# Kernel tuning notes

Hardware: AMD Instinct MI355X
Metric: run time of the kernel (lower is better)

Reference implementation:

```python
import jax, jax.numpy as jnp
import numpy as np

H = 8            # num_heads
EPS = 1e-5       # LayerNorm eps (torch default)
SLOPE = 0.01     # leaky_relu negative slope (torch default)


def layernorm(x, g, b):
    mu = jnp.mean(x, axis=-1, keepdims=True)
    var = jnp.mean((x - mu) ** 2, axis=-1, keepdims=True)
    return (x - mu) * jax.lax.rsqrt(var + EPS) * g + b


def setup_inputs() -> dict:
    key = jax.random.key(0)
    ks = jax.random.split(key, 20)
    B, T, Din, Dh = 4, 2048, 512, 512
    s_in = 1.0 / np.sqrt(Din)
    s_h = 1.0 / np.sqrt(Dh)
    inp = {
        'q': jax.random.normal(ks[0], (B, T, Din), jnp.float32),
        'k': jax.random.normal(ks[1], (B, T, Din), jnp.float32),
        'v': jax.random.normal(ks[2], (B, T, Din), jnp.float32),
        # attention projections (stored as [in, out] for x @ W + b)
        'Wq': jax.random.uniform(ks[3], (Din, Dh), jnp.float32, -s_in, s_in),
        'bq': jax.random.uniform(ks[4], (Dh,), jnp.float32, -s_in, s_in),
        'Wk': jax.random.uniform(ks[5], (Din, Dh), jnp.float32, -s_in, s_in),
        'bk': jax.random.uniform(ks[6], (Dh,), jnp.float32, -s_in, s_in),
        'Wv': jax.random.uniform(ks[7], (Din, Dh), jnp.float32, -s_in, s_in),
        'bv': jax.random.uniform(ks[8], (Dh,), jnp.float32, -s_in, s_in),
        'Wo': jax.random.uniform(ks[9], (Dh, Dh), jnp.float32, -s_h, s_h),
        'bo': jax.random.uniform(ks[10], (Dh,), jnp.float32, -s_h, s_h),
        # FFN
        'Wh': jax.random.uniform(ks[11], (Dh, Dh), jnp.float32, -s_h, s_h),
        'bh': jax.random.uniform(ks[12], (Dh,), jnp.float32, -s_h, s_h),
        'W2': jax.random.uniform(ks[13], (Dh, Dh), jnp.float32, -s_h, s_h),
        'b2': jax.random.uniform(ks[14], (Dh,), jnp.float32, -s_h, s_h),
        # LayerNorms
        'g1': jnp.ones((Dh,), jnp.float32),
        'be1': jnp.zeros((Dh,), jnp.float32),
        'g2': jnp.ones((Dh,), jnp.float32),
        'be2': jnp.zeros((Dh,), jnp.float32),
    }
    return inp


def _block(q, k, v, Wq, bq, Wk, bk, Wv, bv, Wo, bo, Wh, bh, W2, b2, g1, be1, g2, be2):
    B, Tq, _ = q.shape
    Tk = k.shape[1]
    Dh = Wq.shape[1]
    dh = Dh // H
    # projections -> [B, H, T, dh]
    qh = (q @ Wq + bq).reshape(B, Tq, H, dh).transpose(0, 2, 1, 3)
    kh = (k @ Wk + bk).reshape(B, Tk, H, dh).transpose(0, 2, 1, 3)
    vh = (v @ Wv + bv).reshape(B, Tk, H, dh).transpose(0, 2, 1, 3)
    scores = jnp.einsum('bhqd,bhkd->bhqk', qh, kh) / np.sqrt(dh)
    # causal mask: tril with diagonal = Tk - Tq (matches get_causal_mask)
    mask = jnp.tril(jnp.ones((Tq, Tk), bool), k=Tk - Tq)
    scores = jnp.where(mask, scores, -jnp.inf)
    attn = jax.nn.softmax(scores, axis=-1)
    x = jnp.einsum('bhqk,bhkd->bhqd', attn, vh)
    x = x.transpose(0, 2, 1, 3).reshape(B, Tq, Dh)
    h = x @ Wo + bo
    if h.shape == q.shape:
        h = h + q  # residual
    h = layernorm(h, g1, be1)
    y = jax.nn.leaky_relu(h @ Wh + bh, SLOPE) @ W2 + b2
    y = y + h  # residual (shapes always equal here)
    return layernorm(y, g2, be2)


def reference(q, k, v, Wq, bq, Wk, bk, Wv, bv, Wo, bo, Wh, bh, W2, b2, g1, be1, g2, be2):
    return _block(q, k, v, Wq, bq, Wk, bk, Wv, bv, Wo, bo, Wh, bh, W2, b2, g1, be1, g2, be2)
```

## Files before the change

### kernel.cpp

```cpp
#include <hip/hip_runtime.h>
#include <math.h>

#define DIN   512
#define TSEQ  2048
#define BATCH 4
#define NH    8
#define DHEAD 64
#define MTOT  8192

typedef __attribute__((ext_vector_type(8))) __bf16 bf16x8;
typedef __attribute__((ext_vector_type(8))) short  s16x8;
typedef __attribute__((ext_vector_type(4))) float  f32x4;

__device__ __forceinline__ unsigned short f2b(float f) {
  union { float f; unsigned int u; } c; c.f = f;
  unsigned int r = (c.u + 0x7fffu + ((c.u >> 16) & 1u)) >> 16;
  return (unsigned short)r;
}

__device__ __forceinline__ unsigned int pkbf(float a, float b) {
  union { __bf16 h[2]; unsigned int u; } c;
  c.h[0] = (__bf16)a; c.h[1] = (__bf16)b; return c.u;
}

__device__ __forceinline__ f32x4 mfma16(bf16x8 a, bf16x8 b, f32x4 c) {
  return __builtin_amdgcn_mfma_f32_16x16x32_bf16(a, b, c, 0, 0, 0);
}

__device__ __forceinline__ void gload16(const void* gsrc, void* ldsbase) {
  __builtin_amdgcn_global_load_lds(
      (const __attribute__((address_space(1))) unsigned int*)gsrc,
      (__attribute__((address_space(3))) unsigned int*)(unsigned int)(unsigned long long)ldsbase,
      16, 0, 0);
}

#define VMCNT0_BARRIER() do { \
    asm volatile("s_waitcnt vmcnt(0)" ::: "memory"); \
    __builtin_amdgcn_s_barrier(); } while (0)

__global__ __launch_bounds__(256) void cast3_kernel(const float* __restrict__ q,
                                                    const float* __restrict__ k,
                                                    const float* __restrict__ v,
                                                    unsigned short* __restrict__ oq,
                                                    unsigned short* __restrict__ ok,
                                                    unsigned short* __restrict__ ov) {
  const float* in = blockIdx.y == 0 ? q : blockIdx.y == 1 ? k : v;
  unsigned short* out = blockIdx.y == 0 ? oq : blockIdx.y == 1 ? ok : ov;
  int i = (blockIdx.x * 256 + threadIdx.x) * 8;
  float4 a = *(const float4*)(in + i);
  float4 b = *(const float4*)(in + i + 4);
  ushort4 u0, u1;
  u0.x = f2b(a.x); u0.y = f2b(a.y); u0.z = f2b(a.z); u0.w = f2b(a.w);
  u1.x = f2b(b.x); u1.y = f2b(b.y); u1.z = f2b(b.z); u1.w = f2b(b.w);
  *(ushort4*)(out + i) = u0;
  *(ushort4*)(out + i + 4) = u1;
}

__global__ __launch_bounds__(256) void transpose6_kernel(const float* __restrict__ w0,
                                                         const float* __restrict__ w1,
                                                         const float* __restrict__ w2,
                                                         const float* __restrict__ w3,
                                                         const float* __restrict__ w4,
                                                         const float* __restrict__ w5,
                                                         unsigned short* __restrict__ Wt) {
  const float* W;
  switch (blockIdx.z) {
    case 0: W = w0; break; case 1: W = w1; break; case 2: W = w2; break;
    case 3: W = w3; break; case 4: W = w4; break; default: W = w5; break;
  }
  unsigned short* dst = Wt + (size_t)blockIdx.z * 512 * 512;
  __shared__ float tile[32][33];
  int bx = blockIdx.x * 32, by = blockIdx.y * 32;
  int tx = threadIdx.x & 31, ty = threadIdx.x >> 5;
  #pragma unroll
  for (int yy = ty; yy < 32; yy += 8)
    tile[yy][tx] = W[(size_t)(by + yy) * DIN + bx + tx];
  __syncthreads();
  #pragma unroll
  for (int yy = ty; yy < 32; yy += 8)
    dst[(size_t)(bx + yy) * DIN + by + tx] = f2b(tile[tx][yy]);
}

__device__ __forceinline__ void gemm_core(const unsigned short* __restrict__ A,
                                          const unsigned short* __restrict__ Bt,
                                          int m0, int n0,
                                          unsigned short (*Als)[64 * 64],
                                          unsigned short (*Bls)[128 * 64],
                                          f32x4 (*acc)[4]) {
  const int tid = threadIdx.x, lane = tid & 63, w = tid >> 6;
  const int wr = w >> 1, wc = w & 1;
  const int l = lane & 15, g = lane >> 4;
  const int r8 = lane >> 3;
  const int sce = ((lane & 7) ^ r8) * 8;
  const int sxr = (l & 7) * 8;

  #define GSTAGE(buf, k0) do { \
      _Pragma("unroll") \
      for (int i_ = 0; i_ < 2; ++i_) { \
        int ia_ = w * 2 + i_; \
        gload16(A + (size_t)(m0 + ia_ * 8 + r8) * 512 + (k0) + sce, &Als[buf][ia_ * 512]); \
      } \
      _Pragma("unroll") \
      for (int i_ = 0; i_ < 4; ++i_) { \
        int ib_ = w * 4 + i_; \
        gload16(Bt + (size_t)(n0 + ib_ * 8 + r8) * 512 + (k0) + sce, &Bls[buf][ib_ * 512]); \
      } } while (0)

  GSTAGE(0, 0);
  VMCNT0_BARRIER();
  for (int t = 0; t < 8; ++t) {
    int cur = t & 1;
    if (t < 7) GSTAGE(cur ^ 1, (t + 1) * 64);
    #pragma unroll
    for (int kk = 0; kk < 2; ++kk) {
      bf16x8 af[2], bf[4];
      #pragma unroll
      for (int m = 0; m < 2; ++m)
        af[m] = *(const bf16x8*)(&Als[cur][(wr * 32 + m * 16 + l) * 64 + ((kk * 32 + g * 8) ^ sxr)]);
      #pragma unroll
      for (int n = 0; n < 4; ++n)
        bf[n] = *(const bf16x8*)(&Bls[cur][(wc * 64 + n * 16 + l) * 64 + ((kk * 32 + g * 8) ^ sxr)]);
      #pragma unroll
      for (int m = 0; m < 2; ++m)
        #pragma unroll
        for (int n = 0; n < 4; ++n)
          acc[m][n] = mfma16(af[m], bf[n], acc[m][n]);
    }
    VMCNT0_BARRIER();
  }
  #undef GSTAGE
}

enum { EPI_BF16 = 0, EPI_F32RES = 2, EPI_LRELU = 3 };

template <int EPI>
__global__ __launch_bounds__(256) void gemm_kernel(const unsigned short* __restrict__ A,
                                                   const unsigned short* __restrict__ Bt,
                                                   const float* __restrict__ bias,
                                                   const float* __restrict__ res,
                                                   void* __restrict__ out) {
  __shared__ unsigned short Als[2][64 * 64];
  __shared__ unsigned short Bls[2][128 * 64];
  const int lane = threadIdx.x & 63, w = threadIdx.x >> 6;
  const int wr = w >> 1, wc = w & 1;
  const int l = lane & 15, g = lane >> 4;
  const int m0 = blockIdx.x * 64, n0 = blockIdx.y * 128;
  f32x4 acc[2][4] = {};
  gemm_core(A, Bt, m0, n0, Als, Bls, acc);

  #pragma unroll
  for (int m = 0; m < 2; ++m) {
    int grb = m0 + wr * 32 + m * 16 + g * 4;
    #pragma unroll
    for (int n = 0; n < 4; ++n) {
      int gc = n0 + wc * 64 + n * 16 + l;
      float bv = bias[gc];
      #pragma unroll
      for (int r = 0; r < 4; ++r) {
        int gr = grb + r;
        float v = acc[m][n][r] + bv;
        if (EPI == EPI_F32RES) {
          ((float*)out)[(size_t)gr * 512 + gc] = v + res[(size_t)gr * 512 + gc];
        } else if (EPI == EPI_BF16) {
          ((unsigned short*)out)[(size_t)gr * 512 + gc] = f2b(v);
        } else {
          v = v > 0.f ? v : 0.01f * v;
          ((unsigned short*)out)[(size_t)gr * 512 + gc] = f2b(v);
        }
      }
    }
  }
}

__global__ __launch_bounds__(256) void gemm_qkv_kernel(const unsigned short* __restrict__ qb,
                                                       const unsigned short* __restrict__ kb,
                                                       const unsigned short* __restrict__ vb,
                                                       const unsigned short* __restrict__ Wt,
                                                       const float* __restrict__ bq,
                                                       const float* __restrict__ bk,
                                                       const float* __restrict__ bv,
                                                       unsigned short* __restrict__ Qp,
                                                       unsigned short* __restrict__ Kp,
                                                       unsigned short* __restrict__ Vt) {
  __shared__ unsigned short Als[2][64 * 64];
  __shared__ unsigned short Bls[2][128 * 64];
  const int z = blockIdx.z;
  const unsigned short* A = z == 0 ? qb : z == 1 ? kb : vb;
  const unsigned short* B = Wt + (size_t)z * 512 * 512;
  const float* bias = z == 0 ? bq : z == 1 ? bk : bv;
  const int lane = threadIdx.x & 63, w = threadIdx.x >> 6;
  const int wr = w >> 1, wc = w & 1;
  const int l = lane & 15, g = lane >> 4;
  const int m0 = blockIdx.x * 64, n0 = blockIdx.y * 128;
  f32x4 acc[2][4] = {};
  gemm_core(A, B, m0, n0, Als, Bls, acc);

  #pragma unroll
  for (int m = 0; m < 2; ++m) {
    int grb = m0 + wr * 32 + m * 16 + g * 4;
    #pragma unroll
    for (int n = 0; n < 4; ++n) {
      int gc = n0 + wc * 64 + n * 16 + l;
      float bvl = bias[gc];
      #pragma unroll
      for (int r = 0; r < 4; ++r) {
        int gr = grb + r;
        float v = acc[m][n][r] + bvl;
        if (z == 0) {
          Qp[(size_t)gr * 512 + gc] = f2b(v);
        } else if (z == 1) {
          Kp[(size_t)gr * 512 + gc] = f2b(v);
        } else {
          int b = gr >> 11, t = gr & 2047;
          Vt[((size_t)(b * 512 + gc) << 11) + t] = f2b(v);
        }
      }
    }
  }
}

__global__ __launch_bounds__(256) void attn_kernel(const unsigned short* __restrict__ Q,
                                                   const unsigned short* __restrict__ K,
                                                   const unsigned short* __restrict__ Vt,
                                                   unsigned short* __restrict__ O) {
  __shared__ unsigned short Kls[2][64 * 64];
  __shared__ unsigned short Vls[2][64 * 64];
  __shared__ unsigned short Pls[4][16 * 64];
  const int tid = threadIdx.x, lane = tid & 63, w = tid >> 6;
  const int l = lane & 15, g = lane >> 4;
  const int bh = blockIdx.x;
  const int qt = (int)gridDim.y - 1 - (int)blockIdx.y;
  const int b = bh >> 3, h = bh & 7;
  const int sx = (l & 7) * 8;
  const float SC2 = 0.125f * 1.44269504088896340736f;
  const float THR = 64.f;

  const int r8 = lane >> 3;
  const int sce = ((lane & 7) ^ r8) * 8;

  #define STAGEKV(buf, kv0) do { \
      _Pragma("unroll") \
      for (int i_ = 0; i_ < 2; ++i_) { \
        int ii_ = w * 2 + i_; \
        int row_ = ii_ * 8 + r8; \
        gload16(K  + (size_t)(b * 2048 + (kv0) + row_) * 512 + h * 64 + sce, &Kls[buf][ii_ * 512]); \
        gload16(Vt + (size_t)(b * 512 + h * 64 + row_) * 2048 + (kv0) + sce, &Vls[buf][ii_ * 512]); \
      } } while (0)

  const int q0 = qt * 64 + w * 16;
  bf16x8 qf[2];
  #pragma unroll
  for (int kf = 0; kf < 2; ++kf)
    qf[kf] = *(const bf16x8*)(Q + (size_t)(b * 2048 + q0 + l) * 512 + h * 64 + kf * 32 + g * 8);

  bf16x8 vones;
  #pragma unroll
  for (int i = 0; i < 8; ++i) vones[i] = (__bf16)1.0f;

  float mrun = -1e30f;
  f32x4 o[4] = {};
  f32x4 os = {0.f, 0.f, 0.f, 0.f};

  STAGEKV(0, 0);
  VMCNT0_BARRIER();

  for (int s = 0; s <= qt; ++s) {
    int cur = s & 1;
    if (s < qt) STAGEKV(cur ^ 1, (s + 1) * 64);
    int kv0 = s * 64;

    f32x4 st[4];
    #pragma unroll
    for (int t = 0; t < 4; ++t) {
      st[t] = f32x4{0.f, 0.f, 0.f, 0.f};
      #pragma unroll
      for (int kf = 0; kf < 2; ++kf) {
        bf16x8 kfr = *(const bf16x8*)(&Kls[cur][(t * 16 + l) * 64 + ((kf * 32 + g * 8) ^ sx)]);
        st[t] = mfma16(kfr, qf[kf], st[t]);
      }
    }
    if (s == qt) {
      const int qrow = q0 + l;
      #pragma unroll
      for (int t = 0; t < 4; ++t)
        #pragma unroll
        for (int r = 0; r < 4; ++r)
          if (kv0 + t * 16 + g * 4 + r > qrow) st[t][r] = -1e30f;
    }

    float mx = fmaxf(
        fmaxf(fmaxf(fmaxf(st[0][0], st[0][1]), st[0][2]),
              fmaxf(fmaxf(st[0][3], st[1][0]), st[1][1])),
        fmaxf(fmaxf(fmaxf(st[1][2], st[1][3]), st[2][0]),
              fmaxf(fmaxf(st[2][1], st[2][2]), st[2][3])));
    mx = fmaxf(mx, fmaxf(fmaxf(st[3][0], st[3][1]), fmaxf(st[3][2], st[3][3])));
    mx = fmaxf(mx, __shfl_xor(mx, 16, 64));
    mx = fmaxf(mx, __shfl_xor(mx, 32, 64));

    if (!__all(mx <= mrun + THR)) {
      float nm = fmaxf(mrun, mx);
      float alpha = exp2f((mrun - nm) * SC2);
      mrun = nm;
      #pragma unroll
      for (int r = 0; r < 4; ++r) {
        float ar = __shfl(alpha, g * 4 + r, 64);
        #pragma unroll
        for (int n = 0; n < 4; ++n) o[n][r] *= ar;
        os[r] *= ar;
      }
    }

    float mS = mrun * SC2;
    #pragma unroll
    for (int t = 0; t < 4; ++t)
      #pragma unroll
      for (int r = 0; r < 4; ++r)
        st[t][r] = exp2f(fmaf(st[t][r], SC2, -mS));

    #pragma unroll
    for (int t = 0; t < 4; ++t) {
      uint2 u;
      u.x = pkbf(st[t][0], st[t][1]);
      u.y = pkbf(st[t][2], st[t][3]);
      *(uint2*)(&Pls[w][l * 64 + ((t * 16 + g * 4) ^ sx)]) = u;
    }
    #pragma unroll
    for (int kf = 0; kf < 2; ++kf) {
      bf16x8 pa = *(const bf16x8*)(&Pls[w][l * 64 + ((kf * 32 + g * 8) ^ sx)]);
      #pragma unroll
      for (int n = 0; n < 4; ++n) {
        bf16x8 vf = *(const bf16x8*)(&Vls[cur][(n * 16 + l) * 64 + ((kf * 32 + g * 8) ^ sx)]);
        o[n] = mfma16(pa, vf, o[n]);
      }
      os = mfma16(pa, vones, os);
    }

    VMCNT0_BARRIER();
  }

  #pragma unroll
  for (int r = 0; r < 4; ++r) {
    float lir = 1.f / os[r];
    #pragma unroll
    for (int n = 0; n < 4; ++n)
      O[(size_t)(b * 2048 + q0 + g * 4 + r) * 512 + h * 64 + n * 16 + l] =
          f2b(o[n][r] * lir);
  }
  #undef STAGEKV
}

template <int WRITE_BF16>
__global__ __launch_bounds__(256) void ln_kernel(const float* __restrict__ X,
                                                 const float* __restrict__ g,
                                                 const float* __restrict__ be,
                                                 float* __restrict__ Yf,
                                                 unsigned short* __restrict__ Yb) {
  int row = blockIdx.x * 4 + (threadIdx.x >> 6);
  int lane = threadIdx.x & 63;
  const float* x = X + (size_t)row * 512;
  float4 v0 = *(const float4*)(x + lane * 4);
  float4 v1 = *(const float4*)(x + 256 + lane * 4);
  float s = v0.x + v0.y + v0.z + v0.w + v1.x + v1.y + v1.z + v1.w;
  #pragma unroll
  for (int t = 1; t < 64; t <<= 1) s += __shfl_xor(s, t, 64);
  float mu = s * (1.f / 512.f);
  float q = 0.f;
  q += (v0.x - mu) * (v0.x - mu); q += (v0.y - mu) * (v0.y - mu);
  q += (v0.z - mu) * (v0.z - mu); q += (v0.w - mu) * (v0.w - mu);
  q += (v1.x - mu) * (v1.x - mu); q += (v1.y - mu) * (v1.y - mu);
  q += (v1.z - mu) * (v1.z - mu); q += (v1.w - mu) * (v1.w - mu);
  #pragma unroll
  for (int t = 1; t < 64; t <<= 1) q += __shfl_xor(q, t, 64);
  float rstd = rsqrtf(q * (1.f / 512.f) + 1e-5f);

  float4 g0 = *(const float4*)(g + lane * 4);
  float4 g1 = *(const float4*)(g + 256 + lane * 4);
  float4 b0 = *(const float4*)(be + lane * 4);
  float4 b1 = *(const float4*)(be + 256 + lane * 4);
  float4 y0, y1;
  y0.x = (v0.x - mu) * rstd * g0.x + b0.x; y0.y = (v0.y - mu) * rstd * g0.y + b0.y;
  y0.z = (v0.z - mu) * rstd * g0.z + b0.z; y0.w = (v0.w - mu) * rstd * g0.w + b0.w;
  y1.x = (v1.x - mu) * rstd * g1.x + b1.x; y1.y = (v1.y - mu) * rstd * g1.y + b1.y;
  y1.z = (v1.z - mu) * rstd * g1.z + b1.z; y1.w = (v1.w - mu) * rstd * g1.w + b1.w;
  if (Yf) {
    *(float4*)(Yf + (size_t)row * 512 + lane * 4) = y0;
    *(float4*)(Yf + (size_t)row * 512 + 256 + lane * 4) = y1;
  }
  if (WRITE_BF16) {
    ushort4 u0, u1;
    u0.x = f2b(y0.x); u0.y = f2b(y0.y); u0.z = f2b(y0.z); u0.w = f2b(y0.w);
    u1.x = f2b(y1.x); u1.y = f2b(y1.y); u1.z = f2b(y1.z); u1.w = f2b(y1.w);
    *(ushort4*)(Yb + (size_t)row * 512 + lane * 4) = u0;
    *(ushort4*)(Yb + (size_t)row * 512 + 256 + lane * 4) = u1;
  }
}

extern "C" void kernel_launch(void* const* d_in, const int* in_sizes, int n_in,
                              void* d_out, int out_size, void* d_ws, size_t ws_size,
                              hipStream_t stream) {
  const float* q_in = (const float*)d_in[0];
  const float* k_in = (const float*)d_in[1];
  const float* v_in = (const float*)d_in[2];
  const float* Wq = (const float*)d_in[3];  const float* bq = (const float*)d_in[4];
  const float* Wk = (const float*)d_in[5];  const float* bk = (const float*)d_in[6];
  const float* Wv = (const float*)d_in[7];  const float* bv = (const float*)d_in[8];
  const float* Wo = (const float*)d_in[9];  const float* bo = (const float*)d_in[10];
  const float* Wh = (const float*)d_in[11]; const float* bh = (const float*)d_in[12];
  const float* W2 = (const float*)d_in[13]; const float* b2 = (const float*)d_in[14];
  const float* g1 = (const float*)d_in[15]; const float* be1 = (const float*)d_in[16];
  const float* g2 = (const float*)d_in[17]; const float* be2 = (const float*)d_in[18];

  char* ws = (char*)d_ws;
  const size_t MD2 = (size_t)MTOT * 512 * 2;
  const size_t W1  = (size_t)512 * 512 * 2;
  const size_t MD4 = (size_t)MTOT * 512 * 4;
  unsigned short* qb_  = (unsigned short*)(ws);
  unsigned short* kb_  = (unsigned short*)(ws + MD2);
  unsigned short* vb_  = (unsigned short*)(ws + 2 * MD2);
  unsigned short* Qp   = (unsigned short*)(ws + 3 * MD2);
  unsigned short* Kp   = (unsigned short*)(ws + 4 * MD2);
  unsigned short* Vt   = (unsigned short*)(ws + 5 * MD2);
  unsigned short* Wt   = (unsigned short*)(ws + 6 * MD2);
  float*          hy   = (float*)(ws + 6 * MD2 + 6 * W1);
  float*          ln1f = (float*)(ws + 6 * MD2 + 6 * W1 + MD4);
  unsigned short* attn = vb_;
  unsigned short* ln1b = qb_;
  unsigned short* f1   = kb_;

  cast3_kernel<<<dim3(MTOT * 512 / 2048, 3), 256, 0, stream>>>(q_in, k_in, v_in, qb_, kb_, vb_);
  transpose6_kernel<<<dim3(16, 16, 6), 256, 0, stream>>>(Wq, Wk, Wv, Wo, Wh, W2, Wt);

  gemm_qkv_kernel<<<dim3(MTOT / 64, 4, 3), 256, 0, stream>>>(
      qb_, kb_, vb_, Wt, bq, bk, bv, Qp, Kp, Vt);

  attn_kernel<<<dim3(BATCH * NH, 32), 256, 0, stream>>>(Qp, Kp, Vt, attn);

  dim3 gg(MTOT / 64, 4);
  gemm_kernel<EPI_F32RES><<<gg, 256, 0, stream>>>(attn, Wt + 3 * 512 * 512, bo, q_in, hy);
  ln_kernel<1><<<MTOT / 4, 256, 0, stream>>>(hy, g1, be1, ln1f, ln1b);
  gemm_kernel<EPI_LRELU><<<gg, 256, 0, stream>>>(ln1b, Wt + 4 * 512 * 512, bh, nullptr, f1);
  gemm_kernel<EPI_F32RES><<<gg, 256, 0, stream>>>(f1, Wt + 5 * 512 * 512, b2, ln1f, hy);
  ln_kernel<0><<<MTOT / 4, 256, 0, stream>>>(hy, g2, be2, (float*)d_out, nullptr);
}
```

Baseline: 255.9 us.

## Shrink GEMM tiles, keep intermediates in bf16, load V directly from global in attention

GEMM tiles go from 64x128 with K-step 64 to 64x64 with K-step 32, which doubles the grid and cuts LDS use, and the XOR swizzle is removed. Intermediates before and after each LayerNorm are now stored as bf16 instead of fp32, and the second residual reads the bf16 LN1 output, which reduces memory traffic and accuracy. The attention kernel stops staging V through LDS and reads V fragments straight from global memory. Without the swizzle the LDS reads may hit bank conflicts, and the unstaged V loads may stall the MFMA work.

After: 297.0 us. 1.16x slower.

```diff
diff --git a/kernel.cpp b/kernel.cpp
--- a/kernel.cpp
+++ b/kernel.cpp
@@ -16,6 +16,10 @@
   union { float f; unsigned int u; } c; c.f = f;
   unsigned int r = (c.u + 0x7fffu + ((c.u >> 16) & 1u)) >> 16;
   return (unsigned short)r;
+}
+
+__device__ __forceinline__ float b2f(unsigned short u) {
+  union { unsigned int i; float f; } c; c.i = (unsigned int)u << 16; return c.f;
 }
 
 __device__ __forceinline__ unsigned int pkbf(float a, float b) {
@@ -84,88 +88,78 @@
 __device__ __forceinline__ void gemm_core(const unsigned short* __restrict__ A,
                                           const unsigned short* __restrict__ Bt,
                                           int m0, int n0,
-                                          unsigned short (*Als)[64 * 64],
-                                          unsigned short (*Bls)[128 * 64],
-                                          f32x4 (*acc)[4]) {
+                                          unsigned short (*Als)[64 * 32],
+                                          unsigned short (*Bls)[64 * 32],
+                                          f32x4 (*acc)[2]) {
   const int tid = threadIdx.x, lane = tid & 63, w = tid >> 6;
   const int wr = w >> 1, wc = w & 1;
   const int l = lane & 15, g = lane >> 4;
-  const int r8 = lane >> 3;
-  const int sce = ((lane & 7) ^ r8) * 8;
-  const int sxr = (l & 7) * 8;
+  const int srow = lane >> 2;
+  const int sce  = (lane & 3) * 8;
 
   #define GSTAGE(buf, k0) do { \
-      _Pragma("unroll") \
-      for (int i_ = 0; i_ < 2; ++i_) { \
-        int ia_ = w * 2 + i_; \
-        gload16(A + (size_t)(m0 + ia_ * 8 + r8) * 512 + (k0) + sce, &Als[buf][ia_ * 512]); \
-      } \
-      _Pragma("unroll") \
-      for (int i_ = 0; i_ < 4; ++i_) { \
-        int ib_ = w * 4 + i_; \
-        gload16(Bt + (size_t)(n0 + ib_ * 8 + r8) * 512 + (k0) + sce, &Bls[buf][ib_ * 512]); \
-      } } while (0)
+      gload16(A  + (size_t)(m0 + w * 16 + srow) * 512 + (k0) + sce, &Als[buf][w * 512]); \
+      gload16(Bt + (size_t)(n0 + w * 16 + srow) * 512 + (k0) + sce, &Bls[buf][w * 512]); \
+    } while (0)
 
   GSTAGE(0, 0);
   VMCNT0_BARRIER();
-  for (int t = 0; t < 8; ++t) {
+  for (int t = 0; t < 16; ++t) {
     int cur = t & 1;
-    if (t < 7) GSTAGE(cur ^ 1, (t + 1) * 64);
-    #pragma unroll
-    for (int kk = 0; kk < 2; ++kk) {
-      bf16x8 af[2], bf[4];
-      #pragma unroll
-      for (int m = 0; m < 2; ++m)
-        af[m] = *(const bf16x8*)(&Als[cur][(wr * 32 + m * 16 + l) * 64 + ((kk * 32 + g * 8) ^ sxr)]);
-      #pragma unroll
-      for (int n = 0; n < 4; ++n)
-        bf[n] = *(const bf16x8*)(&Bls[cur][(wc * 64 + n * 16 + l) * 64 + ((kk * 32 + g * 8) ^ sxr)]);
-      #pragma unroll
-      for (int m = 0; m < 2; ++m)
-        #pragma unroll
-        for (int n = 0; n < 4; ++n)
-          acc[m][n] = mfma16(af[m], bf[n], acc[m][n]);
-    }
+    if (t < 15) GSTAGE(cur ^ 1, (t + 1) * 32);
+    bf16x8 af[2], bf[2];
+    #pragma unroll
+    for (int m = 0; m < 2; ++m)
+      af[m] = *(const bf16x8*)(&Als[cur][(wr * 32 + m * 16 + l) * 32 + g * 8]);
+    #pragma unroll
+    for (int n = 0; n < 2; ++n)
+      bf[n] = *(const bf16x8*)(&Bls[cur][(wc * 32 + n * 16 + l) * 32 + g * 8]);
+    #pragma unroll
+    for (int m = 0; m < 2; ++m)
+      #pragma unroll
+      for (int n = 0; n < 2; ++n)
+        acc[m][n] = mfma16(af[m], bf[n], acc[m][n]);
     VMCNT0_BARRIER();
   }
   #undef GSTAGE
 }
 
-enum { EPI_BF16 = 0, EPI_F32RES = 2, EPI_LRELU = 3 };
+enum { EPI_BF16 = 0, EPI_VT = 1, EPI_RESF32 = 2, EPI_RESB16 = 3, EPI_LRELU = 4 };
 
 template <int EPI>
 __global__ __launch_bounds__(256) void gemm_kernel(const unsigned short* __restrict__ A,
                                                    const unsigned short* __restrict__ Bt,
                                                    const float* __restrict__ bias,
-                                                   const float* __restrict__ res,
-                                                   void* __restrict__ out) {
-  __shared__ unsigned short Als[2][64 * 64];
-  __shared__ unsigned short Bls[2][128 * 64];
+                                                   const void* __restrict__ res,
+                                                   unsigned short* __restrict__ out) {
+  __shared__ unsigned short Als[2][64 * 32];
+  __shared__ unsigned short Bls[2][64 * 32];
   const int lane = threadIdx.x & 63, w = threadIdx.x >> 6;
   const int wr = w >> 1, wc = w & 1;
   const int l = lane & 15, g = lane >> 4;
-  const int m0 = blockIdx.x * 64, n0 = blockIdx.y * 128;
-  f32x4 acc[2][4] = {};
+  const int m0 = blockIdx.x * 64, n0 = blockIdx.y * 64;
+  f32x4 acc[2][2] = {};
   gemm_core(A, Bt, m0, n0, Als, Bls, acc);
 
   #pragma unroll
   for (int m = 0; m < 2; ++m) {
     int grb = m0 + wr * 32 + m * 16 + g * 4;
     #pragma unroll
-    for (int n = 0; n < 4; ++n) {
-      int gc = n0 + wc * 64 + n * 16 + l;
+    for (int n = 0; n < 2; ++n) {
+      int gc = n0 + wc * 32 + n * 16 + l;
       float bv = bias[gc];
       #pragma unroll
       for (int r = 0; r < 4; ++r) {
         int gr = grb + r;
         float v = acc[m][n][r] + bv;
-        if (EPI == EPI_F32RES) {
-          ((float*)out)[(size_t)gr * 512 + gc] = v + res[(size_t)gr * 512 + gc];
-        } else if (EPI == EPI_BF16) {
-          ((unsigned short*)out)[(size_t)gr * 512 + gc] = f2b(v);
+        if (EPI == EPI_RESF32) v += ((const float*)res)[(size_t)gr * 512 + gc];
+        if (EPI == EPI_RESB16) v += b2f(((const unsigned short*)res)[(size_t)gr * 512 + gc]);
+        if (EPI == EPI_LRELU)  v = v > 0.f ? v : 0.01f * v;
+        if (EPI == EPI_VT) {
+          int b = gr >> 11, t = gr & 2047;
+          out[((size_t)(b * 512 + gc) << 11) + t] = f2b(v);
         } else {
-          v = v > 0.f ? v : 0.01f * v;
-          ((unsigned short*)out)[(size_t)gr * 512 + gc] = f2b(v);
+          out[(size_t)gr * 512 + gc] = f2b(v);
         }
       }
     }
@@ -182,8 +176,8 @@
                                                        unsigned short* __restrict__ Qp,
                                                        unsigned short* __restrict__ Kp,
                                                        unsigned short* __restrict__ Vt) {
-  __shared__ unsigned short Als[2][64 * 64];
-  __shared__ unsigned short Bls[2][128 * 64];
+  __shared__ unsigned short Als[2][64 * 32];
+  __shared__ unsigned short Bls[2][64 * 32];
   const int z = blockIdx.z;
   const unsigned short* A = z == 0 ? qb : z == 1 ? kb : vb;
   const unsigned short* B = Wt + (size_t)z * 512 * 512;
@@ -191,16 +185,16 @@
   const int lane = threadIdx.x & 63, w = threadIdx.x >> 6;
   const int wr = w >> 1, wc = w & 1;
   const int l = lane & 15, g = lane >> 4;
-  const int m0 = blockIdx.x * 64, n0 = blockIdx.y * 128;
-  f32x4 acc[2][4] = {};
+  const int m0 = blockIdx.x * 64, n0 = blockIdx.y * 64;
+  f32x4 acc[2][2] = {};
   gemm_core(A, B, m0, n0, Als, Bls, acc);
 
   #pragma unroll
   for (int m = 0; m < 2; ++m) {
     int grb = m0 + wr * 32 + m * 16 + g * 4;
     #pragma unroll
-    for (int n = 0; n < 4; ++n) {
-      int gc = n0 + wc * 64 + n * 16 + l;
+    for (int n = 0; n < 2; ++n) {
+      int gc = n0 + wc * 32 + n * 16 + l;
       float bvl = bias[gc];
       #pragma unroll
       for (int r = 0; r < 4; ++r) {
@@ -224,7 +218,6 @@
                                                    const unsigned short* __restrict__ Vt,
                                                    unsigned short* __restrict__ O) {
   __shared__ unsigned short Kls[2][64 * 64];
-  __shared__ unsigned short Vls[2][64 * 64];
   __shared__ unsigned short Pls[4][16 * 64];
   const int tid = threadIdx.x, lane = tid & 63, w = tid >> 6;
   const int l = lane & 15, g = lane >> 4;
@@ -238,13 +231,12 @@
   const int r8 = lane >> 3;
   const int sce = ((lane & 7) ^ r8) * 8;
 
-  #define STAGEKV(buf, kv0) do { \
+  #define STAGEK(buf, kv0) do { \
       _Pragma("unroll") \
       for (int i_ = 0; i_ < 2; ++i_) { \
         int ii_ = w * 2 + i_; \
-        int row_ = ii_ * 8 + r8; \
-        gload16(K  + (size_t)(b * 2048 + (kv0) + row_) * 512 + h * 64 + sce, &Kls[buf][ii_ * 512]); \
-        gload16(Vt + (size_t)(b * 512 + h * 64 + row_) * 2048 + (kv0) + sce, &Vls[buf][ii_ * 512]); \
+        gload16(K + (size_t)(b * 2048 + (kv0) + ii_ * 8 + r8) * 512 + h * 64 + sce, \
+                &Kls[buf][ii_ * 512]); \
       } } while (0)
 
   const int q0 = qt * 64 + w * 16;
@@ -261,13 +253,21 @@
   f32x4 o[4] = {};
   f32x4 os = {0.f, 0.f, 0.f, 0.f};
 
-  STAGEKV(0, 0);
+  STAGEK(0, 0);
   VMCNT0_BARRIER();
 
   for (int s = 0; s <= qt; ++s) {
     int cur = s & 1;
-    if (s < qt) STAGEKV(cur ^ 1, (s + 1) * 64);
     int kv0 = s * 64;
+    if (s < qt) STAGEK(cur ^ 1, kv0 + 64);
+
+    bf16x8 vf[2][4];
+    #pragma unroll
+    for (int kf = 0; kf < 2; ++kf)
+      #pragma unroll
+      for (int n = 0; n < 4; ++n)
+        vf[kf][n] = *(const bf16x8*)(
+            Vt + (size_t)(b * 512 + h * 64 + n * 16 + l) * 2048 + kv0 + kf * 32 + g * 8);
 
     f32x4 st[4];
     #pragma unroll
@@ -328,10 +328,8 @@
     for (int kf = 0; kf < 2; ++kf) {
       bf16x8 pa = *(const bf16x8*)(&Pls[w][l * 64 + ((kf * 32 + g * 8) ^ sx)]);
       #pragma unroll
-      for (int n = 0; n < 4; ++n) {
-        bf16x8 vf = *(const bf16x8*)(&Vls[cur][(n * 16 + l) * 64 + ((kf * 32 + g * 8) ^ sx)]);
-        o[n] = mfma16(pa, vf, o[n]);
-      }
+      for (int n = 0; n < 4; ++n)
+        o[n] = mfma16(pa, vf[kf][n], o[n]);
       os = mfma16(pa, vones, os);
     }
 
@@ -346,52 +344,52 @@
       O[(size_t)(b * 2048 + q0 + g * 4 + r) * 512 + h * 64 + n * 16 + l] =
           f2b(o[n][r] * lir);
   }
-  #undef STAGEKV
-}
-
-template <int WRITE_BF16>
-__global__ __launch_bounds__(256) void ln_kernel(const float* __restrict__ X,
-                                                 const float* __restrict__ g,
-                                                 const float* __restrict__ be,
-                                                 float* __restrict__ Yf,
-                                                 unsigned short* __restrict__ Yb) {
+  #undef STAGEK
+}
+
+template <int OUTF32>
+__global__ __launch_bounds__(256) void lnb_kernel(const unsigned short* __restrict__ X,
+                                                  const float* __restrict__ g,
+                                                  const float* __restrict__ be,
+                                                  float* __restrict__ Yf,
+                                                  unsigned short* __restrict__ Yb) {
   int row = blockIdx.x * 4 + (threadIdx.x >> 6);
   int lane = threadIdx.x & 63;
-  const float* x = X + (size_t)row * 512;
-  float4 v0 = *(const float4*)(x + lane * 4);
-  float4 v1 = *(const float4*)(x + 256 + lane * 4);
-  float s = v0.x + v0.y + v0.z + v0.w + v1.x + v1.y + v1.z + v1.w;
+  s16x8 v = *(const s16x8*)(X + (size_t)row * 512 + lane * 8);
+  float f[8];
+  #pragma unroll
+  for (int j = 0; j < 8; ++j) f[j] = b2f((unsigned short)v[j]);
+  float s = 0.f;
+  #pragma unroll
+  for (int j = 0; j < 8; ++j) s += f[j];
   #pragma unroll
   for (int t = 1; t < 64; t <<= 1) s += __shfl_xor(s, t, 64);
   float mu = s * (1.f / 512.f);
   float q = 0.f;
-  q += (v0.x - mu) * (v0.x - mu); q += (v0.y - mu) * (v0.y - mu);
-  q += (v0.z - mu) * (v0.z - mu); q += (v0.w - mu) * (v0.w - mu);
-  q += (v1.x - mu) * (v1.x - mu); q += (v1.y - mu) * (v1.y - mu);
-  q += (v1.z - mu) * (v1.z - mu); q += (v1.w - mu) * (v1.w - mu);
+  #pragma unroll
+  for (int j = 0; j < 8; ++j) q += (f[j] - mu) * (f[j] - mu);
   #pragma unroll
   for (int t = 1; t < 64; t <<= 1) q += __shfl_xor(q, t, 64);
   float rstd = rsqrtf(q * (1.f / 512.f) + 1e-5f);
 
-  float4 g0 = *(const float4*)(g + lane * 4);
-  float4 g1 = *(const float4*)(g + 256 + lane * 4);
-  float4 b0 = *(const float4*)(be + lane * 4);
-  float4 b1 = *(const float4*)(be + 256 + lane * 4);
-  float4 y0, y1;
-  y0.x = (v0.x - mu) * rstd * g0.x + b0.x; y0.y = (v0.y - mu) * rstd * g0.y + b0.y;
-  y0.z = (v0.z - mu) * rstd * g0.z + b0.z; y0.w = (v0.w - mu) * rstd * g0.w + b0.w;
-  y1.x = (v1.x - mu) * rstd * g1.x + b1.x; y1.y = (v1.y - mu) * rstd * g1.y + b1.y;
-  y1.z = (v1.z - mu) * rstd * g1.z + b1.z; y1.w = (v1.w - mu) * rstd * g1.w + b1.w;
-  if (Yf) {
-    *(float4*)(Yf + (size_t)row * 512 + lane * 4) = y0;
-    *(float4*)(Yf + (size_t)row * 512 + 256 + lane * 4) = y1;
-  }
-  if (WRITE_BF16) {
-    ushort4 u0, u1;
-    u0.x = f2b(y0.x); u0.y = f2b(y0.y); u0.z = f2b(y0.z); u0.w = f2b(y0.w);
-    u1.x = f2b(y1.x); u1.y = f2b(y1.y); u1.z = f2b(y1.z); u1.w = f2b(y1.w);
-    *(ushort4*)(Yb + (size_t)row * 512 + lane * 4) = u0;
-    *(ushort4*)(Yb + (size_t)row * 512 + 256 + lane * 4) = u1;
+  float4 g0 = *(const float4*)(g + lane * 8);
+  float4 g1 = *(const float4*)(g + lane * 8 + 4);
+  float4 b0 = *(const float4*)(be + lane * 8);
+  float4 b1 = *(const float4*)(be + lane * 8 + 4);
+  float y[8];
+  y[0] = (f[0] - mu) * rstd * g0.x + b0.x; y[1] = (f[1] - mu) * rstd * g0.y + b0.y;
+  y[2] = (f[2] - mu) * rstd * g0.z + b0.z; y[3] = (f[3] - mu) * rstd * g0.w + b0.w;
+  y[4] = (f[4] - mu) * rstd * g1.x + b1.x; y[5] = (f[5] - mu) * rstd * g1.y + b1.y;
+  y[6] = (f[6] - mu) * rstd * g1.z + b1.z; y[7] = (f[7] - mu) * rstd * g1.w + b1.w;
+  if (OUTF32) {
+    float4 o0 = {y[0], y[1], y[2], y[3]}, o1 = {y[4], y[5], y[6], y[7]};
+    *(float4*)(Yf + (size_t)row * 512 + lane * 8) = o0;
+    *(float4*)(Yf + (size_t)row * 512 + lane * 8 + 4) = o1;
+  } else {
+    uint4 u;
+    u.x = pkbf(y[0], y[1]); u.y = pkbf(y[2], y[3]);
+    u.z = pkbf(y[4], y[5]); u.w = pkbf(y[6], y[7]);
+    *(uint4*)(Yb + (size_t)row * 512 + lane * 8) = u;
   }
 }
 
@@ -413,7 +411,6 @@
   char* ws = (char*)d_ws;
   const size_t MD2 = (size_t)MTOT * 512 * 2;
   const size_t W1  = (size_t)512 * 512 * 2;
-  const size_t MD4 = (size_t)MTOT * 512 * 4;
   unsigned short* qb_  = (unsigned short*)(ws);
   unsigned short* kb_  = (unsigned short*)(ws + MD2);
   unsigned short* vb_  = (unsigned short*)(ws + 2 * MD2);
@@ -421,24 +418,24 @@
   unsigned short* Kp   = (unsigned short*)(ws + 4 * MD2);
   unsigned short* Vt   = (unsigned short*)(ws + 5 * MD2);
   unsigned short* Wt   = (unsigned short*)(ws + 6 * MD2);
-  float*          hy   = (float*)(ws + 6 * MD2 + 6 * W1);
-  float*          ln1f = (float*)(ws + 6 * MD2 + 6 * W1 + MD4);
   unsigned short* attn = vb_;
+  unsigned short* hy   = kb_;
   unsigned short* ln1b = qb_;
-  unsigned short* f1   = kb_;
+  unsigned short* f1   = Qp;
+  unsigned short* y2   = Kp;
 
   cast3_kernel<<<dim3(MTOT * 512 / 2048, 3), 256, 0, stream>>>(q_in, k_in, v_in, qb_, kb_, vb_);
   transpose6_kernel<<<dim3(16, 16, 6), 256, 0, stream>>>(Wq, Wk, Wv, Wo, Wh, W2, Wt);
 
-  gemm_qkv_kernel<<<dim3(MTOT / 64, 4, 3), 256, 0, stream>>>(
+  gemm_qkv_kernel<<<dim3(MTOT / 64, 8, 3), 256, 0, stream>>>(
       qb_, kb_, vb_, Wt, bq, bk, bv, Qp, Kp, Vt);
 
   attn_kernel<<<dim3(BATCH * NH, 32), 256, 0, stream>>>(Qp, Kp, Vt, attn);
 
-  dim3 gg(MTOT / 64, 4);
-  gemm_kernel<EPI_F32RES><<<gg, 256, 0, stream>>>(attn, Wt + 3 * 512 * 512, bo, q_in, hy);
-  ln_kernel<1><<<MTOT / 4, 256, 0, stream>>>(hy, g1, be1, ln1f, ln1b);
+  dim3 gg(MTOT / 64, 8);
+  gemm_kernel<EPI_RESF32><<<gg, 256, 0, stream>>>(attn, Wt + 3 * 512 * 512, bo, q_in, hy);
+  lnb_kernel<0><<<MTOT / 4, 256, 0, stream>>>(hy, g1, be1, nullptr, ln1b);
   gemm_kernel<EPI_LRELU><<<gg, 256, 0, stream>>>(ln1b, Wt + 4 * 512 * 512, bh, nullptr, f1);
-  gemm_kernel<EPI_F32RES><<<gg, 256, 0, stream>>>(f1, Wt + 5 * 512 * 512, b2, ln1f, hy);
-  ln_kernel<0><<<MTOT / 4, 256, 0, stream>>>(hy, g2, be2, (float*)d_out, nullptr);
-}
+  gemm_kernel<EPI_RESB16><<<gg, 256, 0, stream>>>(f1, Wt + 5 * 512 * 512, b2, ln1b, y2);
+  lnb_kernel<1><<<MTOT / 4, 256, 0, stream>>>(y2, g2, be2, (float*)d_out, nullptr);
+}
```
